# Optimization experiments

Hardware: AMD Instinct MI355X
Metric: run time of the kernel (lower is better)

The kernel has to match this reference:

```python
import jax, jax.numpy as jnp
import numpy as np

U, I, D = 60000, 90000, 64
N = U + I
NNZ_R, NNZ_S = 1_000_000, 1_000_000
N_RATINGS = 5
RATING_LAYERS = 2
SOCIAL_LAYERS = 2
EMB_COMB = 1.0


def setup_inputs() -> dict:
    key = jax.random.key(0)
    ks = jax.random.split(key, 24)
    inp = {
        'rating_rows': jax.random.randint(ks[0], (N_RATINGS, NNZ_R), 0, N, dtype=jnp.int32),
        'rating_cols': jax.random.randint(ks[1], (N_RATINGS, NNZ_R), 0, N, dtype=jnp.int32),
        'rating_vals': jax.random.uniform(ks[2], (N_RATINGS, NNZ_R), dtype=jnp.float32),
        'friend_rows': jax.random.randint(ks[3], (NNZ_S,), 0, U, dtype=jnp.int32),
        'friend_cols': jax.random.randint(ks[4], (NNZ_S,), 0, U, dtype=jnp.int32),
        'friend_vals': jax.random.uniform(ks[5], (NNZ_S,), dtype=jnp.float32),
        'group_rows': jax.random.randint(ks[6], (NNZ_S,), 0, U, dtype=jnp.int32),
        'group_cols': jax.random.randint(ks[7], (NNZ_S,), 0, U, dtype=jnp.int32),
        'group_vals': jax.random.uniform(ks[8], (NNZ_S,), dtype=jnp.float32),
        'rating_user_emb': jax.random.normal(ks[9], (N_RATINGS, U, D), dtype=jnp.float32) * 0.1,
        'rating_item_emb': jax.random.normal(ks[10], (N_RATINGS, I, D), dtype=jnp.float32) * 0.1,
        'friend_emb': jax.random.normal(ks[11], (U, D), dtype=jnp.float32) * 0.1,
        'group_emb': jax.random.normal(ks[12], (U, D), dtype=jnp.float32) * 0.1,
        'user_att_w': jax.random.normal(ks[13], (D,), dtype=jnp.float32) * 0.1,
        'user_att_mat_w': jax.random.normal(ks[14], (D, D), dtype=jnp.float32) * 0.1,
        'item_att_w': jax.random.normal(ks[15], (D,), dtype=jnp.float32) * 0.1,
        'item_att_mat_w': jax.random.normal(ks[16], (D, D), dtype=jnp.float32) * 0.1,
        'social_att_w': jax.random.normal(ks[17], (D,), dtype=jnp.float32) * 0.1,
        'social_att_mat_w': jax.random.normal(ks[18], (D, D), dtype=jnp.float32) * 0.1,
        'adaptive_emb_comb': jax.random.uniform(ks[19], (U,), dtype=jnp.float32) + 0.5,
    }
    return inp


def _spmm(rows, cols, vals, x, n):
    # COO sparse matmul: out[r] += vals[e] * x[cols[e]]
    return jax.ops.segment_sum(vals[:, None] * x[cols], rows, num_segments=n)


def _l2norm(x):
    # F.normalize(x, p=2, dim=1)
    return x / jnp.clip(jnp.linalg.norm(x, axis=1, keepdims=True), 1e-12)


def _att_fuse(embs, a, M):
    # embs: [C, N, D]; weight[c,n] = tanh((emb @ M.T) @ a); softmax over channels C
    w = jnp.tanh(jnp.einsum('cnd,ed,e->cn', embs, M, a))
    scores = jax.nn.softmax(w, axis=0)  # [C, N]
    mixed = jnp.einsum('cn,cnd->nd', scores, embs)
    return mixed, scores


def reference(rating_rows, rating_cols, rating_vals,
              friend_rows, friend_cols, friend_vals,
              group_rows, group_cols, group_vals,
              rating_user_emb, rating_item_emb, friend_emb, group_emb,
              user_att_w, user_att_mat_w, item_att_w, item_att_mat_w,
              social_att_w, social_att_mat_w, adaptive_emb_comb):
    # ---- rating channels: LightGCN propagation over bipartite graph ----
    user_list, item_list = [], []
    for c in range(N_RATINGS):
        ego = jnp.concatenate([rating_user_emb[c], rating_item_emb[c]], axis=0)  # [N, D]
        layers = []
        for _ in range(RATING_LAYERS):
            ego = _spmm(rating_rows[c], rating_cols[c], rating_vals[c], ego, N)
            layers.append(ego)
        mean_emb = jnp.mean(jnp.stack(layers, axis=0), axis=0)
        user_list.append(mean_emb[:U])
        item_list.append(mean_emb[U:])
    user_embs = jnp.stack(user_list, axis=0)  # [C, U, D]
    item_embs = jnp.stack(item_list, axis=0)  # [C, I, D]
    mixed_rating_user, user_scores = _att_fuse(user_embs, user_att_w, user_att_mat_w)
    mixed_rating_item, item_scores = _att_fuse(item_embs, item_att_w, item_att_mat_w)

    # ---- social channels: propagation + per-layer L2 normalize ----
    def social_prop(rows, cols, vals, emb):
        outs = []
        for _ in range(SOCIAL_LAYERS):
            emb = _l2norm(_spmm(rows, cols, vals, emb, U))
            outs.append(emb)
        return jnp.mean(jnp.stack(outs, axis=0), axis=0)

    friend_u = social_prop(friend_rows, friend_cols, friend_vals, friend_emb)
    group_u = social_prop(group_rows, group_cols, group_vals, group_emb)
    social_embs = jnp.stack([friend_u, group_u], axis=0)  # [2, U, D]
    mixed_social, social_scores = _att_fuse(social_embs, social_att_w, social_att_mat_w)

    # ---- adaptive combination ----
    num = jnp.sum(mixed_rating_user * mixed_social, axis=1)
    denom = (jnp.clip(jnp.linalg.norm(mixed_rating_user, axis=1), 1e-8)
             * jnp.clip(jnp.linalg.norm(mixed_social, axis=1), 1e-8))
    emb_sim = num / denom
    emb_sim_up_0 = jnp.maximum(emb_sim, 0.0)
    base = (SOCIAL_LAYERS + RATING_LAYERS) / 2.0
    rate = EMB_COMB / (base + emb_sim_up_0 * adaptive_emb_comb)[:, None]  # [U, 1]
    mixed_user = mixed_rating_user + mixed_social * rate
    return (user_scores, item_scores, social_scores, mixed_user, mixed_rating_item)
```

## Files before the change

### kernel.cpp

```cpp
#include <hip/hip_runtime.h>
#include <hip/hip_bf16.h>

#define UU 60000
#define II 90000
#define DD 64
#define NN 150000
#define NNZC 1000000
#define NTOT 7000000
#define MTOT 870000
#define ROW_S0 750000
#define NBR 733
#define NBCK 1046
#define CAPE 8192
#define ACH 16384
#define GRID_A 428
#define ABLK 1024

struct SpmmJob {
    int mode;
    int rowBase;
    int nRows;
    const float* xloF;
    const float* xhiF;
    const uint2* tblB;
    const uint2* selfB;
    uint2* outB;
    float4* outF;
    float* wOut;
};

__device__ __forceinline__ int wave_incl_scan(int x) {
    int lane = threadIdx.x & 63;
#pragma unroll
    for (int d = 1; d < 64; d <<= 1) {
        int y = __shfl_up(x, d, 64);
        if (lane >= d) x += y;
    }
    return x;
}

__device__ int block_incl_scan(int x, int* lds) {
    int wid = threadIdx.x >> 6, lane = threadIdx.x & 63;
    int ws_ = wave_incl_scan(x);
    if (lane == 63) lds[wid] = ws_;
    __syncthreads();
    int off = 0;
    for (int w = 0; w < wid; ++w) off += lds[w];
    __syncthreads();
    return ws_ + off;
}

__device__ __forceinline__ float2 unpack_bf16x2(unsigned p) {
    float2 r;
    r.x = __uint_as_float(p << 16);
    r.y = __uint_as_float(p & 0xffff0000u);
    return r;
}

__device__ __forceinline__ unsigned pack_bf16x2(float a, float b) {
    __hip_bfloat162 h = __float22bfloat162_rn(make_float2(a, b));
    return *(unsigned*)&h;
}

__device__ __forceinline__ uint2 pack4(float4 m) {
    return make_uint2(pack_bf16x2(m.x, m.y), pack_bf16x2(m.z, m.w));
}

__device__ __forceinline__ float4 unpack4(uint2 p) {
    float2 a = unpack_bf16x2(p.x), b = unpack_bf16x2(p.y);
    return make_float4(a.x, a.y, b.x, b.y);
}

__device__ __forceinline__ int bid_of(int grow) {
    return (grow < ROW_S0) ? (grow >> 10) : NBR + (grow - ROW_S0) / 384;
}

__global__ void att_vec_kernel(const float* __restrict__ au, const float* __restrict__ Mu,
                               const float* __restrict__ ai, const float* __restrict__ Mi,
                               const float* __restrict__ as_, const float* __restrict__ Ms,
                               float* __restrict__ v) {
    int d = threadIdx.x;
    float su = 0.f, si = 0.f, ss = 0.f;
    for (int e = 0; e < DD; ++e) {
        su += au[e] * Mu[e * DD + d];
        si += ai[e] * Mi[e * DD + d];
        ss += as_[e] * Ms[e * DD + d];
    }
    v[d] = su;
    v[DD + d] = si;
    v[2 * DD + d] = ss;
}

__device__ __forceinline__ void decode_full(int e, const int* __restrict__ rR,
                                            const int* __restrict__ rC, const float* __restrict__ rV,
                                            const int* __restrict__ fR, const int* __restrict__ fC,
                                            const float* __restrict__ fV,
                                            const int* __restrict__ gR, const int* __restrict__ gC,
                                            const float* __restrict__ gV,
                                            int& grow, int& c, float& v) {
    if (e < 5 * NNZC) { grow = (e / NNZC) * NN + rR[e]; c = rC[e]; v = rV[e]; }
    else if (e < 6 * NNZC) { int k = e - 5 * NNZC; grow = ROW_S0 + fR[k]; c = fC[k]; v = fV[k]; }
    else { int k = e - 6 * NNZC; grow = ROW_S0 + UU + gR[k]; c = gC[k]; v = gV[k]; }
}

__global__ __launch_bounds__(ABLK) void pa_count_kernel(const int* __restrict__ rR,
                                                        const int* __restrict__ fR,
                                                        const int* __restrict__ gR,
                                                        int* __restrict__ gHistT,
                                                        unsigned short* __restrict__ grank) {
    __shared__ int lcnt[NBCK];
    int k = blockIdx.x;
    int cbase = k * ACH;
    int eEnd = min(cbase + ACH, NTOT);
    for (int b = threadIdx.x; b < NBCK; b += ABLK) lcnt[b] = 0;
    __syncthreads();
    for (int e0 = cbase + threadIdx.x; e0 < eEnd; e0 += 4 * ABLK) {
        int gw[4]; bool val[4];
#pragma unroll
        for (int u = 0; u < 4; ++u) {
            int e = e0 + u * ABLK;
            val[u] = e < eEnd;
            int ec = val[u] ? e : cbase;
            if (ec < 5 * NNZC) gw[u] = (ec / NNZC) * NN + rR[ec];
            else if (ec < 6 * NNZC) gw[u] = ROW_S0 + fR[ec - 5 * NNZC];
            else gw[u] = ROW_S0 + UU + gR[ec - 6 * NNZC];
        }
        int rk[4];
#pragma unroll
        for (int u = 0; u < 4; ++u)
            rk[u] = val[u] ? atomicAdd(&lcnt[bid_of(gw[u])], 1) : 0;
#pragma unroll
        for (int u = 0; u < 4; ++u)
            if (val[u]) grank[e0 + u * ABLK] = (unsigned short)rk[u];
    }
    __syncthreads();
    for (int b = threadIdx.x; b < NBCK; b += ABLK)
        gHistT[(size_t)b * GRID_A + k] = lcnt[b];
}

__global__ void kprefix_kernel(int* __restrict__ gHistT, int* __restrict__ bTot) {
    int b = blockIdx.x * (blockDim.x >> 6) + (threadIdx.x >> 6);
    if (b >= NBCK) return;
    int lane = threadIdx.x & 63;
    int* g = gHistT + (size_t)b * GRID_A;
    int carry = 0;
    for (int c0 = 0; c0 < GRID_A; c0 += 64) {
        int idx = c0 + lane;
        int v = (idx < GRID_A) ? g[idx] : 0;
        int incl = wave_incl_scan(v);
        if (idx < GRID_A) g[idx] = carry + incl - v;
        carry += __shfl(incl, 63, 64);
    }
    if (lane == 0) bTot[b] = carry;
}

__global__ void bscan_kernel(const int* __restrict__ bTot, int* __restrict__ bStart,
                             int* __restrict__ rowptr) {
    __shared__ int lds8[8];
    __shared__ int sOff;
    if (threadIdx.x == 0) sOff = 0;
    __syncthreads();
    for (int base = 0; base < NBCK; base += 256) {
        int i = base + threadIdx.x;
        int v = (i < NBCK) ? bTot[i] : 0;
        int incl = block_incl_scan(v, lds8);
        if (i < NBCK) bStart[i] = sOff + incl - v;
        __syncthreads();
        if (threadIdx.x == 255) sOff += incl;
        __syncthreads();
    }
    if (threadIdx.x == 0) { bStart[NBCK] = sOff; rowptr[MTOT] = sOff; }
}

__global__ __launch_bounds__(ABLK) void pa_scatter_kernel(
        const int* __restrict__ rR, const int* __restrict__ rC, const float* __restrict__ rV,
        const int* __restrict__ fR, const int* __restrict__ fC, const float* __restrict__ fV,
        const int* __restrict__ gR, const int* __restrict__ gC, const float* __restrict__ gV,
        const int* __restrict__ bStart, const int* __restrict__ gHistT,
        const unsigned short* __restrict__ grank, uint2* __restrict__ ecv) {
    __shared__ int lcur[NBCK];
    int k = blockIdx.x;
    int cbase = k * ACH;
    int eEnd = min(cbase + ACH, NTOT);
    for (int b = threadIdx.x; b < NBCK; b += ABLK)
        lcur[b] = bStart[b] + gHistT[(size_t)b * GRID_A + k];
    __syncthreads();
    for (int e0 = cbase + threadIdx.x; e0 < eEnd; e0 += 4 * ABLK) {
        int gw[4], cc[4]; float vv[4]; int rk[4]; bool val[4];
#pragma unroll
        for (int u = 0; u < 4; ++u) {
            int e = e0 + u * ABLK;
            val[u] = e < eEnd;
            int ec = val[u] ? e : cbase;
            decode_full(ec, rR, rC, rV, fR, fC, fV, gR, gC, gV, gw[u], cc[u], vv[u]);
            rk[u] = grank[ec];
        }
#pragma unroll
        for (int u = 0; u < 4; ++u) {
            if (!val[u]) continue;
            int pos = lcur[bid_of(gw[u])] + rk[u];
            int lrow = (gw[u] < ROW_S0) ? (gw[u] & 1023) : ((gw[u] - ROW_S0) % 384);
            ecv[pos] = make_uint2(((unsigned)lrow << 18) | (unsigned)cc[u],
                                  __float_as_uint(vv[u]));
        }
    }
}

__global__ __launch_bounds__(256) void phaseB_kernel(const int* __restrict__ bStart,
                                                     int* __restrict__ rowptr,
                                                     const uint2* __restrict__ ecv,
                                                     uint2* __restrict__ edata) {
    __shared__ unsigned short perm[CAPE];
    __shared__ int off[1024];
    __shared__ int lds8[8];
    int b = blockIdx.x;
    int firstRow = (b < NBR) ? (b << 10) : ROW_S0 + (b - NBR) * 384;
    int rowEnd = (b < NBR) ? min((b + 1) << 10, ROW_S0)
                           : min(ROW_S0 + (b - NBR + 1) * 384, MTOT);
    int nRows = rowEnd - firstRow;
    int dst = bStart[b];
    int count = bStart[b + 1] - dst;
    for (int i = threadIdx.x; i < nRows; i += 256) off[i] = 0;
    __syncthreads();
    for (int i = threadIdx.x; i < count; i += 256)
        atomicAdd(&off[ecv[dst + i].x >> 18], 1);
    __syncthreads();
    int base4 = threadIdx.x * 4;
    int v4[4], s = 0;
#pragma unroll
    for (int kk = 0; kk < 4; ++kk) {
        int i = base4 + kk;
        v4[kk] = (i < nRows) ? off[i] : 0;
        s += v4[kk];
    }
    int incl = block_incl_scan(s, lds8);
    int run = incl - s;
#pragma unroll
    for (int kk = 0; kk < 4; ++kk) {
        int i = base4 + kk;
        if (i < nRows) { rowptr[firstRow + i] = dst + run; off[i] = run; }
        run += v4[kk];
    }
    __syncthreads();
    if (count <= CAPE) {
        for (int i = threadIdx.x; i < count; i += 256) {
            int pos = atomicAdd(&off[ecv[dst + i].x >> 18], 1);
            perm[pos] = (unsigned short)i;
        }
        __syncthreads();
        for (int i = threadIdx.x; i < count; i += 256) {
            uint2 e = ecv[dst + perm[i]];
            edata[dst + i] = make_uint2(e.x & 0x3FFFFu, e.y);
        }
    } else {
        for (int i = threadIdx.x; i < count; i += 256) {
            uint2 e = ecv[dst + i];
            int pos = atomicAdd(&off[e.x >> 18], 1);
            edata[dst + pos] = make_uint2(e.x & 0x3FFFFu, e.y);
        }
    }
}

template <int MODE>
__device__ __forceinline__ void spmm_body(int blk, const SpmmJob& j,
                                          const int* __restrict__ rowptr,
                                          const uint2* __restrict__ edata,
                                          const float* __restrict__ vvec) {
    int lane = threadIdx.x & 63;
    int l16 = lane & 15;
    int grpBase = lane & 48;
    int wid = blk * (int)(blockDim.x >> 6) + (threadIdx.x >> 6);
    int row = wid * 4 + (lane >> 4);
    bool active = row < j.nRows;
    int g = j.rowBase + row;
    int start = active ? rowptr[g] : 0;
    int end = active ? rowptr[g + 1] : 0;
    float4 acc = make_float4(0.f, 0.f, 0.f, 0.f);
    for (int j0 = start; j0 < end; j0 += 16) {
        uint2 md = make_uint2(0u, 0u);
        if (j0 + l16 < end) md = edata[j0 + l16];
        int cnt = min(end - j0, 16);
        for (int js = 0; js < cnt; js += 8) {
            int cc[8]; float vv[8]; float4 xv[8];
#pragma unroll
            for (int u = 0; u < 8; ++u) {
                int jj = js + u;
                int sl = grpBase + ((jj < cnt) ? jj : 0);
                cc[u] = __shfl((int)md.x, sl, 64);
                float v = __uint_as_float((unsigned)__shfl((int)md.y, sl, 64));
                vv[u] = (jj < cnt) ? v : 0.f;
            }
#pragma unroll
            for (int u = 0; u < 8; ++u) {
                int c = cc[u];
                if (MODE == 0) {
                    const float* src = (c < UU) ? (j.xloF + (size_t)c * DD)
                                                : (j.xhiF + (size_t)(c - UU) * DD);
                    xv[u] = *(const float4*)(src + 4 * l16);
                } else if (MODE == 2) {
                    xv[u] = *(const float4*)(j.xloF + (size_t)c * DD + 4 * l16);
                } else {
                    xv[u] = unpack4(j.tblB[(size_t)c * 16 + l16]);
                }
            }
#pragma unroll
            for (int u = 0; u < 8; ++u) {
                acc.x += vv[u] * xv[u].x; acc.y += vv[u] * xv[u].y;
                acc.z += vv[u] * xv[u].z; acc.w += vv[u] * xv[u].w;
            }
        }
    }
    if (!active) return;
    size_t ro = (size_t)row * 16 + l16;
    if (MODE == 0) {
        j.outB[ro] = pack4(acc);
    } else if (MODE == 1) {
        float4 sv = unpack4(j.selfB[ro]);
        float4 m = make_float4(0.5f * (acc.x + sv.x), 0.5f * (acc.y + sv.y),
                               0.5f * (acc.z + sv.z), 0.5f * (acc.w + sv.w));
        j.outB[ro] = pack4(m);
        const float* vv = (row < UU) ? vvec : (vvec + DD);
        float4 vw = *(const float4*)(vv + 4 * l16);
        float p = m.x * vw.x + m.y * vw.y + m.z * vw.z + m.w * vw.w;
        p += __shfl_xor(p, 1, 64); p += __shfl_xor(p, 2, 64);
        p += __shfl_xor(p, 4, 64); p += __shfl_xor(p, 8, 64);
        if (l16 == 0) j.wOut[row] = tanhf(p);
    } else if (MODE == 2) {
        float n2 = acc.x * acc.x + acc.y * acc.y + acc.z * acc.z + acc.w * acc.w;
        n2 += __shfl_xor(n2, 1, 64); n2 += __shfl_xor(n2, 2, 64);
        n2 += __shfl_xor(n2, 4, 64); n2 += __shfl_xor(n2, 8, 64);
        float inv = 1.f / fmaxf(sqrtf(n2), 1e-12f);
        j.outB[ro] = pack4(make_float4(acc.x * inv, acc.y * inv, acc.z * inv, acc.w * inv));
    } else {
        float n2 = acc.x * acc.x + acc.y * acc.y + acc.z * acc.z + acc.w * acc.w;
        n2 += __shfl_xor(n2, 1, 64); n2 += __shfl_xor(n2, 2, 64);
        n2 += __shfl_xor(n2, 4, 64); n2 += __shfl_xor(n2, 8, 64);
        float inv = 1.f / fmaxf(sqrtf(n2), 1e-12f);
        float4 sv = unpack4(j.selfB[ro]);
        j.outF[ro] = make_float4(0.5f * (sv.x + acc.x * inv), 0.5f * (sv.y + acc.y * inv),
                                 0.5f * (sv.z + acc.z * inv), 0.5f * (sv.w + acc.w * inv));
    }
}

template <int MODE>
__global__ __launch_bounds__(256) void spmm_kernel(SpmmJob j, const int* __restrict__ rowptr,
                                                   const uint2* __restrict__ edata,
                                                   const float* __restrict__ vvec) {
    spmm_body<MODE>(blockIdx.x, j, rowptr, edata, vvec);
}

__global__ __launch_bounds__(256) void spmm_dual_kernel(SpmmJob a, int aBlocks, SpmmJob b,
                                                        const int* __restrict__ rowptr,
                                                        const uint2* __restrict__ edata,
                                                        const float* __restrict__ vvec) {
    SpmmJob j;
    int blk;
    if ((int)blockIdx.x < aBlocks) { j = a; blk = blockIdx.x; }
    else { j = b; blk = blockIdx.x - aBlocks; }
    switch (j.mode) {
        case 0: spmm_body<0>(blk, j, rowptr, edata, vvec); break;
        case 1: spmm_body<1>(blk, j, rowptr, edata, vvec); break;
        case 2: spmm_body<2>(blk, j, rowptr, edata, vvec); break;
        default: spmm_body<3>(blk, j, rowptr, edata, vvec); break;
    }
}

__global__ __launch_bounds__(256) void mix_social_kernel(
        const __hip_bfloat16* __restrict__ chanEmb, const float* __restrict__ w,
        float* __restrict__ oUS, float* __restrict__ oIS,
        float* __restrict__ mixedRU, float* __restrict__ oMI, int nMix,
        SpmmJob s0, int s0Blocks, SpmmJob s1,
        const int* __restrict__ rowptr, const uint2* __restrict__ edata,
        const float* __restrict__ vvec) {
    if ((int)blockIdx.x >= nMix) {
        int r = blockIdx.x - nMix;
        if (r < s0Blocks) spmm_body<2>(r, s0, rowptr, edata, vvec);
        else spmm_body<2>(r - s0Blocks, s1, rowptr, edata, vvec);
        return;
    }
    int lane = threadIdx.x & 63;
    int n = blockIdx.x * 4 + (threadIdx.x >> 6);
    if (n >= NN) return;
    float sw[5];
    float mx = -2.0f;
#pragma unroll
    for (int c = 0; c < 5; ++c) {
        sw[c] = w[(size_t)c * NN + n];
        mx = fmaxf(mx, sw[c]);
    }
    float sum = 0.f;
#pragma unroll
    for (int c = 0; c < 5; ++c) {
        sw[c] = expf(sw[c] - mx);
        sum += sw[c];
    }
    float inv = 1.0f / sum;
    float acc = 0.f;
#pragma unroll
    for (int c = 0; c < 5; ++c) {
        sw[c] *= inv;
        acc += sw[c] * __bfloat162float(chanEmb[((size_t)c * NN + n) * DD + lane]);
    }
    if (n < UU) {
#pragma unroll
        for (int c = 0; c < 5; ++c)
            if (lane == c) oUS[(size_t)c * UU + n] = sw[c];
        mixedRU[(size_t)n * DD + lane] = acc;
    } else {
        int m = n - UU;
#pragma unroll
        for (int c = 0; c < 5; ++c)
            if (lane == c) oIS[(size_t)c * II + m] = sw[c];
        oMI[(size_t)m * DD + lane] = acc;
    }
}

__global__ __launch_bounds__(256) void social2_kernel(SpmmJob s0, int s0Blocks, SpmmJob s1,
                                                      const int* __restrict__ rowptr,
                                                      const uint2* __restrict__ edata,
                                                      const float* __restrict__ vvec) {
    if ((int)blockIdx.x < s0Blocks) spmm_body<3>(blockIdx.x, s0, rowptr, edata, vvec);
    else spmm_body<3>(blockIdx.x - s0Blocks, s1, rowptr, edata, vvec);
}

__global__ void social_mix_final_kernel(const float* __restrict__ e0, const float* __restrict__ e1,
                                        const float* __restrict__ vs,
                                        const float* __restrict__ mixedRU,
                                        const float* __restrict__ adaptive,
                                        float* __restrict__ scoresOut,
                                        float* __restrict__ outMU) {
    int lane = threadIdx.x & 63;
    int n = blockIdx.x * (blockDim.x >> 6) + (threadIdx.x >> 6);
    if (n >= UU) return;
    size_t idx = (size_t)n * DD + lane;
    float a = e0[idx];
    float b = e1[idx];
    float v = vs[lane];
    float pa = a * v, pb = b * v;
    float mru = mixedRU[idx];
#pragma unroll
    for (int m = 32; m >= 1; m >>= 1) { pa += __shfl_xor(pa, m, 64); pb += __shfl_xor(pb, m, 64); }
    float w0 = tanhf(pa);
    float w1 = tanhf(pb);
    float mx = fmaxf(w0, w1);
    float x0 = expf(w0 - mx);
    float x1 = expf(w1 - mx);
    float invs = 1.0f / (x0 + x1);
    float s0 = x0 * invs;
    float s1 = x1 * invs;
    if (lane == 0) {
        scoresOut[n] = s0;
        scoresOut[UU + n] = s1;
    }
    float ms = s0 * a + s1 * b;
    float nm = mru * ms, na2 = mru * mru, nb2 = ms * ms;
#pragma unroll
    for (int m = 32; m >= 1; m >>= 1) {
        nm += __shfl_xor(nm, m, 64); na2 += __shfl_xor(na2, m, 64); nb2 += __shfl_xor(nb2, m, 64);
    }
    float denom = fmaxf(sqrtf(na2), 1e-8f) * fmaxf(sqrtf(nb2), 1e-8f);
    float sim = nm / denom;
    float rate = 1.0f / (2.0f + fmaxf(sim, 0.f) * adaptive[n]);
    outMU[idx] = mru + ms * rate;
}

extern "C" void kernel_launch(void* const* d_in, const int* in_sizes, int n_in,
                              void* d_out, int out_size, void* d_ws, size_t ws_size,
                              hipStream_t stream) {
    const int* r_rows = (const int*)d_in[0];
    const int* r_cols = (const int*)d_in[1];
    const float* r_vals = (const float*)d_in[2];
    const int* f_rows = (const int*)d_in[3];
    const int* f_cols = (const int*)d_in[4];
    const float* f_vals = (const float*)d_in[5];
    const int* g_rows = (const int*)d_in[6];
    const int* g_cols = (const int*)d_in[7];
    const float* g_vals = (const float*)d_in[8];
    const float* rue = (const float*)d_in[9];
    const float* rie = (const float*)d_in[10];
    const float* femb = (const float*)d_in[11];
    const float* gemb = (const float*)d_in[12];
    const float* uaw = (const float*)d_in[13];
    const float* uamw = (const float*)d_in[14];
    const float* iaw = (const float*)d_in[15];
    const float* iamw = (const float*)d_in[16];
    const float* saw = (const float*)d_in[17];
    const float* samw = (const float*)d_in[18];
    const float* adapt = (const float*)d_in[19];

    float* ws = (float*)d_ws;
    size_t o = 0;
    int* rowptr = (int*)(ws + o); o += 870016;
    int* bStart = (int*)(ws + o); o += 2048;
    int* bTot   = (int*)(ws + o); o += 2048;
    int* gHistT = (int*)(ws + o); o += 448000;
    float* R1 = ws + o; o += 14000000;
    float* edF = ws + o; o += 14000000;
    float* R2 = ws + o; o += 24000000;
    float* wrat = ws + o; o += 750016;
    float* vvec = ws + o; o += 192;
    float* socF = ws + o; o += 3840000;

    uint2* ecv = (uint2*)R1;
    uint2* edata = (uint2*)edF;
    unsigned short* grank = (unsigned short*)R2;
    uint2* AtmpB0 = (uint2*)R1;
    uint2* AtmpB1 = AtmpB0 + (size_t)NN * 16;
    float* mixedRU = R1;
    float* socM0 = R1 + 4800000;
    float* socM1 = R1 + 8640000;
    __hip_bfloat16* chanMean = (__hip_bfloat16*)R2;
    uint2* socL1B0 = (uint2*)socF;
    uint2* socL1B1 = socL1B0 + (size_t)UU * 16;

    float* out = (float*)d_out;
    float* oUS = out;
    float* oIS = oUS + (size_t)5 * UU;
    float* oSS = oIS + (size_t)5 * II;
    float* oMU = oSS + (size_t)2 * UU;
    float* oMI = oMU + (size_t)UU * DD;

    const dim3 blk(256);
    const dim3 blkA(ABLK);
    const int gridN4 = (NN + 15) / 16;
    const int gridU4 = (UU + 15) / 16;
    const int gridMix = (NN + 3) / 4;
    const int gridFin = (UU + 3) / 4;

    att_vec_kernel<<<1, 64, 0, stream>>>(uaw, uamw, iaw, iamw, saw, samw, vvec);

    pa_count_kernel<<<GRID_A, blkA, 0, stream>>>(r_rows, f_rows, g_rows, gHistT, grank);
    kprefix_kernel<<<(NBCK + 3) / 4, blk, 0, stream>>>(gHistT, bTot);
    bscan_kernel<<<1, blk, 0, stream>>>(bTot, bStart, rowptr);
    pa_scatter_kernel<<<GRID_A, blkA, 0, stream>>>(r_rows, r_cols, r_vals,
                                                   f_rows, f_cols, f_vals,
                                                   g_rows, g_cols, g_vals,
                                                   bStart, gHistT, grank, ecv);
    phaseB_kernel<<<NBCK, blk, 0, stream>>>(bStart, rowptr, ecv, edata);

    auto jobL1 = [&](int c) {
        SpmmJob j{};
        j.mode = 0; j.rowBase = c * NN; j.nRows = NN;
        j.xloF = rue + (size_t)c * UU * DD;
        j.xhiF = rie + (size_t)c * II * DD;
        j.outB = (c & 1) ? AtmpB1 : AtmpB0;
        return j;
    };
    auto jobL2 = [&](int c) {
        SpmmJob j{};
        j.mode = 1; j.rowBase = c * NN; j.nRows = NN;
        j.tblB = (c & 1) ? AtmpB1 : AtmpB0;
        j.selfB = j.tblB;
        j.outB = (uint2*)(chanMean + (size_t)c * NN * DD);
        j.wOut = wrat + (size_t)c * NN;
        return j;
    };
    spmm_kernel<0><<<gridN4, blk, 0, stream>>>(jobL1(0), rowptr, edata, vvec);
    for (int c = 1; c < 5; ++c)
        spmm_dual_kernel<<<2 * gridN4, blk, 0, stream>>>(jobL1(c), gridN4, jobL2(c - 1),
                                                         rowptr, edata, vvec);
    spmm_kernel<1><<<gridN4, blk, 0, stream>>>(jobL2(4), rowptr, edata, vvec);

    SpmmJob sf1{}; sf1.mode = 2; sf1.rowBase = ROW_S0; sf1.nRows = UU;
    sf1.xloF = femb; sf1.outB = socL1B0;
    SpmmJob sg1{}; sg1.mode = 2; sg1.rowBase = ROW_S0 + UU; sg1.nRows = UU;
    sg1.xloF = gemb; sg1.outB = socL1B1;
    mix_social_kernel<<<gridMix + 2 * gridU4, blk, 0, stream>>>(
        chanMean, wrat, oUS, oIS, mixedRU, oMI, gridMix,
        sf1, gridU4, sg1, rowptr, edata, vvec);

    SpmmJob sf2{}; sf2.mode = 3; sf2.rowBase = ROW_S0; sf2.nRows = UU;
    sf2.tblB = socL1B0; sf2.selfB = socL1B0; sf2.outF = (float4*)socM0;
    SpmmJob sg2{}; sg2.mode = 3; sg2.rowBase = ROW_S0 + UU; sg2.nRows = UU;
    sg2.tblB = socL1B1; sg2.selfB = socL1B1; sg2.outF = (float4*)socM1;
    social2_kernel<<<2 * gridU4, blk, 0, stream>>>(sf2, gridU4, sg2, rowptr, edata, vvec);

    social_mix_final_kernel<<<gridFin, blk, 0, stream>>>(socM0, socM1, vvec + 2 * DD,
                                                         mixedRU, adapt, oSS, oMU);
}
```

Measured before the change: 664.6 us.

## Pre-convert fp32 embedding tables to bf16 in piggybacked blocks for SpMM gathers

Adds a conversion pass that packs each fp32 rating and social embedding table into a bf16 gather table. The conversion blocks ride along in earlier kernels (scatter, phaseB and the fused SpMM launches) so they overlap with other work. All SpMM layers then gather half-width rows instead of fp32 rows. The workspace is re-laid out to hold the extra tables, and the mix and social-layer-1 work is split into separate launches. This trades extra conversion traffic and precision for smaller random gathers, and it adds launches and workspace aliasing risk.

```diff
diff --git a/kernel.cpp b/kernel.cpp
--- a/kernel.cpp
+++ b/kernel.cpp
@@ -20,8 +20,6 @@
     int mode;
     int rowBase;
     int nRows;
-    const float* xloF;
-    const float* xhiF;
     const uint2* tblB;
     const uint2* selfB;
     uint2* outB;
@@ -29,6 +27,14 @@
     float* wOut;
 };
 
+struct CvtJob {
+    const float* lo;
+    const float* hi;
+    uint2* dst;
+    int nRows;
+    int split;
+};
+
 __device__ __forceinline__ int wave_incl_scan(int x) {
     int lane = threadIdx.x & 63;
 #pragma unroll
@@ -73,6 +79,18 @@
 
 __device__ __forceinline__ int bid_of(int grow) {
     return (grow < ROW_S0) ? (grow >> 10) : NBR + (grow - ROW_S0) / 384;
+}
+
+__device__ __forceinline__ void cvt_body(int blk, int nblks, const CvtJob& cv) {
+    int total = cv.nRows * 16;
+    int stride = nblks * (int)blockDim.x;
+    for (int i = blk * (int)blockDim.x + (int)threadIdx.x; i < total; i += stride) {
+        int row = i >> 4, h = i & 15;
+        const float* src = (row < cv.split) ? (cv.lo + (size_t)row * DD)
+                                            : (cv.hi + (size_t)(row - cv.split) * DD);
+        float4 x = *(const float4*)(src + 4 * h);
+        cv.dst[i] = pack4(x);
+    }
 }
 
 __global__ void att_vec_kernel(const float* __restrict__ au, const float* __restrict__ Mu,
@@ -177,7 +195,12 @@
         const int* __restrict__ fR, const int* __restrict__ fC, const float* __restrict__ fV,
         const int* __restrict__ gR, const int* __restrict__ gC, const float* __restrict__ gV,
         const int* __restrict__ bStart, const int* __restrict__ gHistT,
-        const unsigned short* __restrict__ grank, uint2* __restrict__ ecv) {
+        const unsigned short* __restrict__ grank, uint2* __restrict__ ecv,
+        CvtJob cv, int cvB) {
+    if ((int)blockIdx.x >= GRID_A) {
+        cvt_body(blockIdx.x - GRID_A, cvB, cv);
+        return;
+    }
     __shared__ int lcur[NBCK];
     int k = blockIdx.x;
     int cbase = k * ACH;
@@ -209,7 +232,12 @@
 __global__ __launch_bounds__(256) void phaseB_kernel(const int* __restrict__ bStart,
                                                      int* __restrict__ rowptr,
                                                      const uint2* __restrict__ ecv,
-                                                     uint2* __restrict__ edata) {
+                                                     uint2* __restrict__ edata,
+                                                     CvtJob cv, int cvB) {
+    if ((int)blockIdx.x >= NBCK) {
+        cvt_body(blockIdx.x - NBCK, cvB, cv);
+        return;
+    }
     __shared__ unsigned short perm[CAPE];
     __shared__ int off[1024];
     __shared__ int lds8[8];
@@ -291,18 +319,8 @@
                 vv[u] = (jj < cnt) ? v : 0.f;
             }
 #pragma unroll
-            for (int u = 0; u < 8; ++u) {
-                int c = cc[u];
-                if (MODE == 0) {
-                    const float* src = (c < UU) ? (j.xloF + (size_t)c * DD)
-                                                : (j.xhiF + (size_t)(c - UU) * DD);
-                    xv[u] = *(const float4*)(src + 4 * l16);
-                } else if (MODE == 2) {
-                    xv[u] = *(const float4*)(j.xloF + (size_t)c * DD + 4 * l16);
-                } else {
-                    xv[u] = unpack4(j.tblB[(size_t)c * 16 + l16]);
-                }
-            }
+            for (int u = 0; u < 8; ++u)
+                xv[u] = unpack4(j.tblB[(size_t)cc[u] * 16 + l16]);
 #pragma unroll
             for (int u = 0; u < 8; ++u) {
                 acc.x += vv[u] * xv[u].x; acc.y += vv[u] * xv[u].y;
@@ -342,21 +360,10 @@
     }
 }
 
-template <int MODE>
-__global__ __launch_bounds__(256) void spmm_kernel(SpmmJob j, const int* __restrict__ rowptr,
-                                                   const uint2* __restrict__ edata,
-                                                   const float* __restrict__ vvec) {
-    spmm_body<MODE>(blockIdx.x, j, rowptr, edata, vvec);
-}
-
-__global__ __launch_bounds__(256) void spmm_dual_kernel(SpmmJob a, int aBlocks, SpmmJob b,
-                                                        const int* __restrict__ rowptr,
-                                                        const uint2* __restrict__ edata,
-                                                        const float* __restrict__ vvec) {
-    SpmmJob j;
-    int blk;
-    if ((int)blockIdx.x < aBlocks) { j = a; blk = blockIdx.x; }
-    else { j = b; blk = blockIdx.x - aBlocks; }
+__device__ __forceinline__ void spmm_run(const SpmmJob& j, int blk,
+                                         const int* __restrict__ rowptr,
+                                         const uint2* __restrict__ edata,
+                                         const float* __restrict__ vvec) {
     switch (j.mode) {
         case 0: spmm_body<0>(blk, j, rowptr, edata, vvec); break;
         case 1: spmm_body<1>(blk, j, rowptr, edata, vvec); break;
@@ -365,21 +372,24 @@
     }
 }
 
-__global__ __launch_bounds__(256) void mix_social_kernel(
-        const __hip_bfloat16* __restrict__ chanEmb, const float* __restrict__ w,
-        float* __restrict__ oUS, float* __restrict__ oIS,
-        float* __restrict__ mixedRU, float* __restrict__ oMI, int nMix,
-        SpmmJob s0, int s0Blocks, SpmmJob s1,
-        const int* __restrict__ rowptr, const uint2* __restrict__ edata,
-        const float* __restrict__ vvec) {
-    if ((int)blockIdx.x >= nMix) {
-        int r = blockIdx.x - nMix;
-        if (r < s0Blocks) spmm_body<2>(r, s0, rowptr, edata, vvec);
-        else spmm_body<2>(r - s0Blocks, s1, rowptr, edata, vvec);
-        return;
-    }
+__global__ __launch_bounds__(256) void fused_kernel(SpmmJob a, int aB, SpmmJob b, int bB,
+                                                    CvtJob cv, int cvB,
+                                                    const int* __restrict__ rowptr,
+                                                    const uint2* __restrict__ edata,
+                                                    const float* __restrict__ vvec) {
+    int bx = blockIdx.x;
+    if (bx < aB) { spmm_run(a, bx, rowptr, edata, vvec); return; }
+    bx -= aB;
+    if (bx < bB) { spmm_run(b, bx, rowptr, edata, vvec); return; }
+    cvt_body(bx - bB, cvB, cv);
+}
+
+__global__ void mix5_kernel(const __hip_bfloat16* __restrict__ chanEmb,
+                            const float* __restrict__ w,
+                            float* __restrict__ oUS, float* __restrict__ oIS,
+                            float* __restrict__ mixedRU, float* __restrict__ oMI) {
     int lane = threadIdx.x & 63;
-    int n = blockIdx.x * 4 + (threadIdx.x >> 6);
+    int n = blockIdx.x * (blockDim.x >> 6) + (threadIdx.x >> 6);
     if (n >= NN) return;
     float sw[5];
     float mx = -2.0f;
@@ -413,14 +423,6 @@
             if (lane == c) oIS[(size_t)c * II + m] = sw[c];
         oMI[(size_t)m * DD + lane] = acc;
     }
-}
-
-__global__ __launch_bounds__(256) void social2_kernel(SpmmJob s0, int s0Blocks, SpmmJob s1,
-                                                      const int* __restrict__ rowptr,
-                                                      const uint2* __restrict__ edata,
-                                                      const float* __restrict__ vvec) {
-    if ((int)blockIdx.x < s0Blocks) spmm_body<3>(blockIdx.x, s0, rowptr, edata, vvec);
-    else spmm_body<3>(blockIdx.x - s0Blocks, s1, rowptr, edata, vvec);
 }
 
 __global__ void social_mix_final_kernel(const float* __restrict__ e0, const float* __restrict__ e1,
@@ -489,29 +491,32 @@
     const float* adapt = (const float*)d_in[19];
 
     float* ws = (float*)d_ws;
-    size_t o = 0;
-    int* rowptr = (int*)(ws + o); o += 870016;
-    int* bStart = (int*)(ws + o); o += 2048;
-    int* bTot   = (int*)(ws + o); o += 2048;
-    int* gHistT = (int*)(ws + o); o += 448000;
-    float* R1 = ws + o; o += 14000000;
-    float* edF = ws + o; o += 14000000;
-    float* R2 = ws + o; o += 24000000;
-    float* wrat = ws + o; o += 750016;
-    float* vvec = ws + o; o += 192;
-    float* socF = ws + o; o += 3840000;
-
-    uint2* ecv = (uint2*)R1;
-    uint2* edata = (uint2*)edF;
-    unsigned short* grank = (unsigned short*)R2;
+    int* rowptr = (int*)ws;
+    int* bStart = rowptr + 870016;
+    int* bTot   = bStart + 2048;
+    int* gHistT = bTot + 2048;
+    float* ED   = ws + 1322112;
+    float* R1   = ED + 14000000;
+    float* CM   = R1 + 11520000;
+    float* tbl0F= CM + 24000000;
+    float* wrat = tbl0F + 4800000;
+    float* vvec = wrat + 750016;
+
+    uint2* edata = (uint2*)ED;
     uint2* AtmpB0 = (uint2*)R1;
     uint2* AtmpB1 = AtmpB0 + (size_t)NN * 16;
     float* mixedRU = R1;
-    float* socM0 = R1 + 4800000;
-    float* socM1 = R1 + 8640000;
-    __hip_bfloat16* chanMean = (__hip_bfloat16*)R2;
-    uint2* socL1B0 = (uint2*)socF;
-    uint2* socL1B1 = socL1B0 + (size_t)UU * 16;
+    float* socM0 = R1 + 3840000;
+    float* socM1 = R1 + 7680000;
+    unsigned short* grank = (unsigned short*)CM;
+    uint2* ecv = (uint2*)(CM + 3500000);
+    __hip_bfloat16* chanMean = (__hip_bfloat16*)CM;
+    uint2* tbl1 = (uint2*)(CM + 19200000);
+    uint2* socL1B0 = (uint2*)CM;
+    uint2* socL1B1 = (uint2*)(CM + 1920000);
+    uint2* tbl0 = (uint2*)tbl0F;
+    uint2* socB0 = (uint2*)tbl0F;
+    uint2* socB1 = socB0 + (size_t)UU * 16;
 
     float* out = (float*)d_out;
     float* oUS = out;
@@ -526,23 +531,36 @@
     const int gridU4 = (UU + 15) / 16;
     const int gridMix = (NN + 3) / 4;
     const int gridFin = (UU + 3) / 4;
+    const int CVB = 2048;
+    const int CVB_A = 512;
+
+    uint2* tblOf[2] = {tbl0, tbl1};
+    auto cvtRating = [&](int c) {
+        CvtJob cv{};
+        cv.lo = rue + (size_t)c * UU * DD;
+        cv.hi = rie + (size_t)c * II * DD;
+        cv.dst = tblOf[c & 1];
+        cv.nRows = NN; cv.split = UU;
+        return cv;
+    };
+    CvtJob cvNone{};
+    cvNone.lo = rue; cvNone.hi = rie; cvNone.dst = tbl0; cvNone.nRows = 0; cvNone.split = UU;
 
     att_vec_kernel<<<1, 64, 0, stream>>>(uaw, uamw, iaw, iamw, saw, samw, vvec);
 
     pa_count_kernel<<<GRID_A, blkA, 0, stream>>>(r_rows, f_rows, g_rows, gHistT, grank);
     kprefix_kernel<<<(NBCK + 3) / 4, blk, 0, stream>>>(gHistT, bTot);
     bscan_kernel<<<1, blk, 0, stream>>>(bTot, bStart, rowptr);
-    pa_scatter_kernel<<<GRID_A, blkA, 0, stream>>>(r_rows, r_cols, r_vals,
-                                                   f_rows, f_cols, f_vals,
-                                                   g_rows, g_cols, g_vals,
-                                                   bStart, gHistT, grank, ecv);
-    phaseB_kernel<<<NBCK, blk, 0, stream>>>(bStart, rowptr, ecv, edata);
+    pa_scatter_kernel<<<GRID_A + CVB_A, blkA, 0, stream>>>(
+        r_rows, r_cols, r_vals, f_rows, f_cols, f_vals, g_rows, g_cols, g_vals,
+        bStart, gHistT, grank, ecv, cvtRating(0), CVB_A);
+    phaseB_kernel<<<NBCK + CVB, blk, 0, stream>>>(bStart, rowptr, ecv, edata,
+                                                  cvtRating(1), CVB);
 
     auto jobL1 = [&](int c) {
         SpmmJob j{};
         j.mode = 0; j.rowBase = c * NN; j.nRows = NN;
-        j.xloF = rue + (size_t)c * UU * DD;
-        j.xhiF = rie + (size_t)c * II * DD;
+        j.tblB = tblOf[c & 1];
         j.outB = (c & 1) ? AtmpB1 : AtmpB0;
         return j;
     };
@@ -555,25 +573,36 @@
         j.wOut = wrat + (size_t)c * NN;
         return j;
     };
-    spmm_kernel<0><<<gridN4, blk, 0, stream>>>(jobL1(0), rowptr, edata, vvec);
-    for (int c = 1; c < 5; ++c)
-        spmm_dual_kernel<<<2 * gridN4, blk, 0, stream>>>(jobL1(c), gridN4, jobL2(c - 1),
-                                                         rowptr, edata, vvec);
-    spmm_kernel<1><<<gridN4, blk, 0, stream>>>(jobL2(4), rowptr, edata, vvec);
+    SpmmJob jNone{}; jNone.mode = 0; jNone.nRows = 0; jNone.tblB = tbl0; jNone.outB = AtmpB0;
+
+    fused_kernel<<<gridN4, blk, 0, stream>>>(jobL1(0), gridN4, jNone, 0, cvNone, 0,
+                                             rowptr, edata, vvec);
+    for (int c = 1; c <= 3; ++c)
+        fused_kernel<<<2 * gridN4 + CVB, blk, 0, stream>>>(
+            jobL1(c), gridN4, jobL2(c - 1), gridN4, cvtRating(c + 1), CVB,
+            rowptr, edata, vvec);
+    fused_kernel<<<2 * gridN4, blk, 0, stream>>>(jobL1(4), gridN4, jobL2(3), gridN4,
+                                                 cvNone, 0, rowptr, edata, vvec);
+    CvtJob cvSoc{};
+    cvSoc.lo = femb; cvSoc.hi = gemb; cvSoc.dst = socB0; cvSoc.nRows = 2 * UU; cvSoc.split = UU;
+    fused_kernel<<<gridN4 + CVB, blk, 0, stream>>>(jobL2(4), gridN4, jNone, 0, cvSoc, CVB,
+                                                   rowptr, edata, vvec);
+
+    mix5_kernel<<<gridMix, blk, 0, stream>>>(chanMean, wrat, oUS, oIS, mixedRU, oMI);
 
     SpmmJob sf1{}; sf1.mode = 2; sf1.rowBase = ROW_S0; sf1.nRows = UU;
-    sf1.xloF = femb; sf1.outB = socL1B0;
+    sf1.tblB = socB0; sf1.outB = socL1B0;
     SpmmJob sg1{}; sg1.mode = 2; sg1.rowBase = ROW_S0 + UU; sg1.nRows = UU;
-    sg1.xloF = gemb; sg1.outB = socL1B1;
-    mix_social_kernel<<<gridMix + 2 * gridU4, blk, 0, stream>>>(
-        chanMean, wrat, oUS, oIS, mixedRU, oMI, gridMix,
-        sf1, gridU4, sg1, rowptr, edata, vvec);
+    sg1.tblB = socB1; sg1.outB = socL1B1;
+    fused_kernel<<<2 * gridU4, blk, 0, stream>>>(sf1, gridU4, sg1, gridU4, cvNone, 0,
+                                                 rowptr, edata, vvec);
 
     SpmmJob sf2{}; sf2.mode = 3; sf2.rowBase = ROW_S0; sf2.nRows = UU;
     sf2.tblB = socL1B0; sf2.selfB = socL1B0; sf2.outF = (float4*)socM0;
     SpmmJob sg2{}; sg2.mode = 3; sg2.rowBase = ROW_S0 + UU; sg2.nRows = UU;
     sg2.tblB = socL1B1; sg2.selfB = socL1B1; sg2.outF = (float4*)socM1;
-    social2_kernel<<<2 * gridU4, blk, 0, stream>>>(sf2, gridU4, sg2, rowptr, edata, vvec);
+    fused_kernel<<<2 * gridU4, blk, 0, stream>>>(sf2, gridU4, sg2, gridU4, cvNone, 0,
+                                                 rowptr, edata, vvec);
 
     social_mix_final_kernel<<<gridFin, blk, 0, stream>>>(socM0, socM1, vvec + 2 * DD,
                                                          mixedRU, adapt, oSS, oMU);
```

After: 604.6 us. 1.1x faster.
